# Kernel optimization log

Hardware: AMD Instinct MI355X
Metric: run time of the kernel (lower is better)

The kernel has to match this reference:

```python
import jax, jax.numpy as jnp
import numpy as np

N_SUBS = 64
INPUT_DIMS = 256
MIDDLE_DIMS = 128
OUTPUT_DIMS = 256
N = 131072


def setup_inputs() -> dict:
    key = jax.random.key(0)
    k1, k2 = jax.random.split(key)
    x = jax.random.normal(k1, (N, INPUT_DIMS), dtype=jnp.float32)
    sub = jax.random.randint(k2, (N,), 0, N_SUBS, dtype=jnp.int64 if jax.config.jax_enable_x64 else jnp.int32)
    # learned scalar params, initialized as in the torch module
    Gamma = jnp.ones((1,), jnp.float32) / (MIDDLE_DIMS * INPUT_DIMS)
    Lambda = jnp.ones((1,), jnp.float32) / (OUTPUT_DIMS * (INPUT_DIMS + MIDDLE_DIMS))
    return {"x": x, "sub": sub, "Gamma": Gamma, "Lambda": Lambda}


def reference(x, sub, Gamma, Lambda):
    # per-subject mean via fused segment reduction (replaces python loop)
    sums = jax.ops.segment_sum(x, sub, num_segments=N_SUBS)                      # [S, D_in]
    counts = jax.ops.segment_sum(jnp.ones((x.shape[0],), x.dtype), sub,
                                 num_segments=N_SUBS)[:, None]                    # [S, 1]
    # torch fallback for empty group: mean over row 0 of x
    means = jnp.where(counts > 0, sums / jnp.maximum(counts, 1), x[0][None, :])   # [S, D_in]
    # F.linear with rank-1 all-Gamma weight == Gamma * row-sum broadcast to middle dims
    s = jax.nn.relu(Gamma[0] * jnp.sum(means, axis=1, keepdims=True))             # [S, 1]
    stats = jnp.broadcast_to(s, (N_SUBS, MIDDLE_DIMS))                            # [S, D_mid]
    batch_stats = stats[sub]                                                      # [N, D_mid] gather
    cat = jnp.concatenate([x, batch_stats], axis=1)                               # [N, D_in+D_mid]
    o = jax.nn.relu(Lambda[0] * jnp.sum(cat, axis=1, keepdims=True))              # [N, 1]
    return jnp.broadcast_to(o, (x.shape[0], OUTPUT_DIMS))                         # [N, D_out]
```

## Files before the change

### kernel.cpp

```cpp
#include <hip/hip_runtime.h>

#define N_ROWS   131072
#define D_IN     256
#define D_MID    128
#define N_SUBS   64


__global__ __launch_bounds__(256) void k1_rowsum(const float* __restrict__ x,
                                                 float* __restrict__ rowsum,
                                                 float* __restrict__ bins) {
    if (blockIdx.x == 0 && threadIdx.x < 2 * N_SUBS) bins[threadIdx.x] = 0.0f;
    int row  = blockIdx.x * 4 + (threadIdx.x >> 6);
    int lane = threadIdx.x & 63;
    const float4* xr = (const float4*)(x + (size_t)row * D_IN);
    float4 v = xr[lane];
    float s = (v.x + v.y) + (v.z + v.w);
    #pragma unroll
    for (int m = 32; m >= 1; m >>= 1) s += __shfl_xor(s, m, 64);
    if (lane == 0) rowsum[row] = s;
}

__global__ __launch_bounds__(256) void k2_group(const float* __restrict__ rowsum,
                                                const int* __restrict__ sub,
                                                float* __restrict__ gsum,
                                                float* __restrict__ gcnt) {
    __shared__ float ls[N_SUBS];
    __shared__ float lc[N_SUBS];
    if (threadIdx.x < N_SUBS) { ls[threadIdx.x] = 0.0f; lc[threadIdx.x] = 0.0f; }
    __syncthreads();
    int stride = gridDim.x * blockDim.x;
    for (int i = blockIdx.x * blockDim.x + threadIdx.x; i < N_ROWS; i += stride) {
        int g = sub[i];
        atomicAdd(&ls[g], rowsum[i]);
        atomicAdd(&lc[g], 1.0f);
    }
    __syncthreads();
    if (threadIdx.x < N_SUBS) {
        atomicAdd(&gsum[threadIdx.x], ls[threadIdx.x]);
        atomicAdd(&gcnt[threadIdx.x], lc[threadIdx.x]);
    }
}

__global__ __launch_bounds__(256) void k3_out(const float* __restrict__ rowsum,
                                              const int* __restrict__ sub,
                                              const float* __restrict__ gsum,
                                              const float* __restrict__ gcnt,
                                              const float* __restrict__ Gamma,
                                              const float* __restrict__ Lambda,
                                              float* __restrict__ out) {
    int row  = blockIdx.x * 4 + (threadIdx.x >> 6);
    int lane = threadIdx.x & 63;
    int g = sub[row];
    float c = gcnt[g];
    float meansum = (c > 0.0f) ? (gsum[g] / c) : rowsum[0];
    float s = Gamma[0] * meansum;
    s = s > 0.0f ? s : 0.0f;
    float o = Lambda[0] * (rowsum[row] + (float)D_MID * s);
    o = o > 0.0f ? o : 0.0f;
    float4 v = make_float4(o, o, o, o);
    ((float4*)(out + (size_t)row * D_IN))[lane] = v;
}

extern "C" void kernel_launch(void* const* d_in, const int* in_sizes, int n_in,
                              void* d_out, int out_size, void* d_ws, size_t ws_size,
                              hipStream_t stream) {
    const float* x      = (const float*)d_in[0];
    const int*   sub    = (const int*)d_in[1];
    const float* Gamma  = (const float*)d_in[2];
    const float* Lambda = (const float*)d_in[3];
    float* out = (float*)d_out;

    float* rowsum = (float*)d_ws;
    float* gsum   = rowsum + N_ROWS;
    float* gcnt   = gsum + N_SUBS;

    k1_rowsum<<<N_ROWS / 4, 256, 0, stream>>>(x, rowsum, gsum);
    k2_group<<<64, 256, 0, stream>>>(rowsum, sub, gsum, gcnt);
    k3_out<<<N_ROWS / 4, 256, 0, stream>>>(rowsum, sub, gsum, gcnt, Gamma, Lambda, out);
}
```

Before: 245.1 us.

## Fuse group binning into rowsum kernel and merge group finalize into output kernel

Row sums and per-subject sum/count bins are computed together in one kernel, with per-block LDS partials written to workspace. A second kernel has every block re-reduce all partials to get per-group terms, then writes the broadcast output with grid-stride waves. This removes the separate global-atomic grouping kernel and one launch. In exchange, each output block redundantly reads the full partials array.

```diff
diff --git a/kernel.cpp b/kernel.cpp
--- a/kernel.cpp
+++ b/kernel.cpp
@@ -5,60 +5,95 @@
 #define D_MID    128
 #define N_SUBS   64
 
+#define K1_BLOCKS      2048
+#define K1_THREADS     256
+#define K1_WAVES       (K1_BLOCKS * K1_THREADS / 64)
+#define K1_ROWS_PER_W  (N_ROWS / K1_WAVES)
 
-__global__ __launch_bounds__(256) void k1_rowsum(const float* __restrict__ x,
-                                                 float* __restrict__ rowsum,
-                                                 float* __restrict__ bins) {
-    if (blockIdx.x == 0 && threadIdx.x < 2 * N_SUBS) bins[threadIdx.x] = 0.0f;
-    int row  = blockIdx.x * 4 + (threadIdx.x >> 6);
+#define K2_BLOCKS      256
+#define K2_THREADS     1024
+#define K2_WAVES       (K2_BLOCKS * K2_THREADS / 64)
+#define K2_ROWS_PER_W  (N_ROWS / K2_WAVES)
+
+
+__global__ __launch_bounds__(256) void k1_rowsum_bins(const float* __restrict__ x,
+                                                      const int* __restrict__ sub,
+                                                      float* __restrict__ rowsum,
+                                                      float* __restrict__ partials) {
+    __shared__ float ls[2 * N_SUBS];
+    if (threadIdx.x < 2 * N_SUBS) ls[threadIdx.x] = 0.0f;
+    __syncthreads();
+
+    int wave = (blockIdx.x * K1_THREADS + threadIdx.x) >> 6;
     int lane = threadIdx.x & 63;
-    const float4* xr = (const float4*)(x + (size_t)row * D_IN);
-    float4 v = xr[lane];
-    float s = (v.x + v.y) + (v.z + v.w);
-    #pragma unroll
-    for (int m = 32; m >= 1; m >>= 1) s += __shfl_xor(s, m, 64);
-    if (lane == 0) rowsum[row] = s;
+
+    #pragma unroll 4
+    for (int r = 0; r < K1_ROWS_PER_W; ++r) {
+        int row = wave + r * K1_WAVES;
+        float4 v = ((const float4*)(x + (size_t)row * D_IN))[lane];
+        float s = (v.x + v.y) + (v.z + v.w);
+        #pragma unroll
+        for (int m = 32; m >= 1; m >>= 1) s += __shfl_xor(s, m, 64);
+        if (lane == 0) {
+            rowsum[row] = s;
+            int g = sub[row];
+            atomicAdd(&ls[g], s);
+            atomicAdd(&ls[N_SUBS + g], 1.0f);
+        }
+    }
+    __syncthreads();
+    if (threadIdx.x < 2 * N_SUBS)
+        partials[(size_t)blockIdx.x * (2 * N_SUBS) + threadIdx.x] = ls[threadIdx.x];
 }
 
-__global__ __launch_bounds__(256) void k2_group(const float* __restrict__ rowsum,
-                                                const int* __restrict__ sub,
-                                                float* __restrict__ gsum,
-                                                float* __restrict__ gcnt) {
-    __shared__ float ls[N_SUBS];
-    __shared__ float lc[N_SUBS];
-    if (threadIdx.x < N_SUBS) { ls[threadIdx.x] = 0.0f; lc[threadIdx.x] = 0.0f; }
-    __syncthreads();
-    int stride = gridDim.x * blockDim.x;
-    for (int i = blockIdx.x * blockDim.x + threadIdx.x; i < N_ROWS; i += stride) {
-        int g = sub[i];
-        atomicAdd(&ls[g], rowsum[i]);
-        atomicAdd(&lc[g], 1.0f);
+__global__ __launch_bounds__(1024) void k2_out(const float* __restrict__ rowsum,
+                                               const int* __restrict__ sub,
+                                               const float* __restrict__ partials,
+                                               const float* __restrict__ Gamma,
+                                               const float* __restrict__ Lambda,
+                                               float* __restrict__ out) {
+    __shared__ float red[8][2 * N_SUBS];
+    __shared__ float tg[N_SUBS];
+    int tid = threadIdx.x;
+
+    {
+        int slot  = tid & 127;
+        int chunk = tid >> 7;
+        float acc = 0.0f;
+        int b0 = chunk * (K1_BLOCKS / 8);
+        for (int b = b0; b < b0 + (K1_BLOCKS / 8); ++b)
+            acc += partials[(size_t)b * (2 * N_SUBS) + slot];
+        red[chunk][slot] = acc;
     }
     __syncthreads();
-    if (threadIdx.x < N_SUBS) {
-        atomicAdd(&gsum[threadIdx.x], ls[threadIdx.x]);
-        atomicAdd(&gcnt[threadIdx.x], lc[threadIdx.x]);
+    if (tid < 2 * N_SUBS) {
+        float t0 = 0.0f;
+        #pragma unroll
+        for (int c = 0; c < 8; ++c) t0 += red[c][tid];
+        red[0][tid] = t0;
     }
-}
+    __syncthreads();
+    if (tid < N_SUBS) {
+        float sum = red[0][tid];
+        float cnt = red[0][N_SUBS + tid];
+        float meansum = (cnt > 0.0f) ? (sum / cnt) : rowsum[0];
+        float s = Gamma[0] * meansum;
+        s = s > 0.0f ? s : 0.0f;
+        tg[tid] = Lambda[0] * (float)D_MID * s;
+    }
+    __syncthreads();
 
-__global__ __launch_bounds__(256) void k3_out(const float* __restrict__ rowsum,
-                                              const int* __restrict__ sub,
-                                              const float* __restrict__ gsum,
-                                              const float* __restrict__ gcnt,
-                                              const float* __restrict__ Gamma,
-                                              const float* __restrict__ Lambda,
-                                              float* __restrict__ out) {
-    int row  = blockIdx.x * 4 + (threadIdx.x >> 6);
-    int lane = threadIdx.x & 63;
-    int g = sub[row];
-    float c = gcnt[g];
-    float meansum = (c > 0.0f) ? (gsum[g] / c) : rowsum[0];
-    float s = Gamma[0] * meansum;
-    s = s > 0.0f ? s : 0.0f;
-    float o = Lambda[0] * (rowsum[row] + (float)D_MID * s);
-    o = o > 0.0f ? o : 0.0f;
-    float4 v = make_float4(o, o, o, o);
-    ((float4*)(out + (size_t)row * D_IN))[lane] = v;
+    float lam  = Lambda[0];
+    int gw   = (blockIdx.x * K2_THREADS + tid) >> 6;
+    int lane = tid & 63;
+
+    #pragma unroll 4
+    for (int r = 0; r < K2_ROWS_PER_W; ++r) {
+        int row = gw + r * K2_WAVES;
+        float o = lam * rowsum[row] + tg[sub[row]];
+        o = o > 0.0f ? o : 0.0f;
+        ((float4*)(out + (size_t)row * D_IN))[lane] = make_float4(o, o, o, o);
+    }
 }
 
 extern "C" void kernel_launch(void* const* d_in, const int* in_sizes, int n_in,
@@ -70,11 +105,9 @@
     const float* Lambda = (const float*)d_in[3];
     float* out = (float*)d_out;
 
-    float* rowsum = (float*)d_ws;
-    float* gsum   = rowsum + N_ROWS;
-    float* gcnt   = gsum + N_SUBS;
+    float* rowsum   = (float*)d_ws;
+    float* partials = rowsum + N_ROWS;
 
-    k1_rowsum<<<N_ROWS / 4, 256, 0, stream>>>(x, rowsum, gsum);
-    k2_group<<<64, 256, 0, stream>>>(rowsum, sub, gsum, gcnt);
-    k3_out<<<N_ROWS / 4, 256, 0, stream>>>(rowsum, sub, gsum, gcnt, Gamma, Lambda, out);
+    k1_rowsum_bins<<<K1_BLOCKS, K1_THREADS, 0, stream>>>(x, sub, rowsum, partials);
+    k2_out<<<K2_BLOCKS, K2_THREADS, 0, stream>>>(rowsum, sub, partials, Gamma, Lambda, out);
 }
```

New measurement: 269.9 us. 10.1% more time.
